# Optimization experiments

Hardware: AMD Instinct MI355X
Metric: run time of the kernel (lower is better)

The kernel has to match this reference:

```python
import jax, jax.numpy as jnp
import numpy as np

K = 100
TEMPERATURE = 0.1


def setup_inputs() -> dict:
    key = jax.random.key(0)
    k1, k2 = jax.random.split(key)
    x = jax.random.normal(k1, (8, 128, 60, 60), dtype=jnp.float32)
    W = jax.random.normal(k2, (128, 2 * K), dtype=jnp.float32) * 0.02  # torch Linear(k*2, d_model).weight
    b = jnp.zeros((128,), dtype=jnp.float32)
    return {"x": x, "W": W, "b": b}


def reference(x, W, b):
    x0, x1 = jnp.split(x, 2, axis=0)
    n, c, h, w = x0.shape
    hw = h * w
    # n c h w -> n (h w) c
    f0 = jnp.transpose(x0.reshape(n, c, hw), (0, 2, 1))
    f1 = jnp.transpose(x1.reshape(n, c, hw), (0, 2, 1))
    # (f0/sqrt(c)) @ (f1/sqrt(c))^T / T  ==  f0 @ f1^T / (c*T)
    sm = jnp.einsum('nld,nsd->nls', f0, f1) / (c * TEMPERATURE)
    cm = (jax.nn.softmax(sm, axis=1) * jax.nn.softmax(sm, axis=2)).reshape(n, hw * hw)
    _, topi = jax.lax.top_k(cm, K)  # (n, K)
    qindex = topi // hw
    rindex = topi % hw
    coords0 = jnp.stack([qindex % w, qindex // w], axis=-1).astype(jnp.float32) / w  # (n, K, 2) as (x, y)
    coords1 = jnp.stack([rindex % w, rindex // w], axis=-1).astype(jnp.float32) / w
    # create_meshgrid(h, w, normalized=False): (1, h*w, 2) with (x, y), row-major
    gy, gx = jnp.meshgrid(jnp.arange(h), jnp.arange(w), indexing='ij')
    grid = jnp.stack([gx, gy], axis=-1).reshape(1, hw, 2).astype(jnp.float32) / w
    offsets0 = grid[:, :, None, :] - coords0[:, None, :, :]  # (n, hw, K, 2)
    offsets1 = grid[:, :, None, :] - coords1[:, None, :, :]
    emb0 = offsets0.reshape(n, hw, 2 * K) @ W.T + b  # (n, hw, d_model)
    emb1 = offsets1.reshape(n, hw, 2 * K) @ W.T + b
    f0 = f0 + emb0
    f1 = f1 + emb1
    f = jnp.concatenate([f0, f1], axis=0)  # (2n, hw, d)
    # n (h w) d -> n d h w
    return jnp.transpose(f, (0, 2, 1)).reshape(2 * n, c, h, w)
```

## Files before the change

kernel.cpp:

```cpp
#include <hip/hip_runtime.h>

#define HW 3600
#define PADR 3712
#define NF4 900
#define CAP 16384
#define KSEL 100
#define NT 58
typedef unsigned long long U64;

using short8   = __attribute__((ext_vector_type(8))) short;
using float4v  = __attribute__((ext_vector_type(4))) float;
using float16v = __attribute__((ext_vector_type(16))) float;

__device__ __forceinline__ unsigned monof(float f) {
    unsigned b = __float_as_uint(f);
    return (b & 0x80000000u) ? ~b : (b | 0x80000000u);
}
__device__ __forceinline__ float unmonof(unsigned m) {
    return __uint_as_float((m & 0x80000000u) ? (m ^ 0x80000000u) : ~m);
}
__device__ __forceinline__ unsigned short f2bf(float f) {
    unsigned b = __float_as_uint(f);
    return (unsigned short)((b + 0x7FFFu + ((b >> 16) & 1u)) >> 16);
}
__device__ __forceinline__ float bf2f(unsigned short h) {
    return __uint_as_float(((unsigned)h) << 16);
}
__device__ __forceinline__ void async16(const void* g, void* l) {
    __builtin_amdgcn_global_load_lds((const __attribute__((address_space(1))) void*)g,
                                     (__attribute__((address_space(3))) void*)l, 16, 0, 0);
}


__global__ __launch_bounds__(256) void conv_k(
    const float* __restrict__ x,
    unsigned short* __restrict__ hiT, unsigned short* __restrict__ loT)
{
    int b = blockIdx.z, l0 = blockIdx.x * 64, d0 = blockIdx.y * 64;
    __shared__ float t[64][65];
    int tid = threadIdx.x;
#pragma unroll
    for (int r = 0; r < 4; r++) {
        int idx = tid + 256 * r;
        int d = idx >> 4, lq = idx & 15;
        int l = l0 + lq * 4;
        const float* src = x + ((size_t)b * 128 + d0 + d) * HW;
        float4 v;
        if (l + 3 < HW) v = *(const float4*)(src + l);
        else {
            v.x = (l     < HW) ? src[l]     : 0.f;
            v.y = (l + 1 < HW) ? src[l + 1] : 0.f;
            v.z = (l + 2 < HW) ? src[l + 2] : 0.f;
            v.w = (l + 3 < HW) ? src[l + 3] : 0.f;
        }
        t[lq * 4 + 0][d] = v.x; t[lq * 4 + 1][d] = v.y;
        t[lq * 4 + 2][d] = v.z; t[lq * 4 + 3][d] = v.w;
    }
    __syncthreads();
    const int rblk = l0 >> 7;
#pragma unroll
    for (int r = 0; r < 2; r++) {
        int idx = tid + 256 * r;
        int l = idx >> 3, dq = idx & 7;
        unsigned hp[4], lp[4];
#pragma unroll
        for (int j = 0; j < 4; j++) {
            float f0 = t[l][dq * 8 + 2 * j], f1 = t[l][dq * 8 + 2 * j + 1];
            unsigned short h0 = f2bf(f0), h1 = f2bf(f1);
            unsigned short g0 = f2bf(f0 - bf2f(h0)), g1 = f2bf(f1 - bf2f(h1));
            hp[j] = (unsigned)h0 | ((unsigned)h1 << 16);
            lp[j] = (unsigned)g0 | ((unsigned)g1 << 16);
        }
        size_t o = ((size_t)(b * 29 + rblk) * 16 + (d0 >> 3) + dq) * 1024
                 + (size_t)((l0 + l) & 127) * 8;
        *(uint4*)(hiT + o) = make_uint4(hp[0], hp[1], hp[2], hp[3]);
        *(uint4*)(loT + o) = make_uint4(lp[0], lp[1], lp[2], lp[3]);
    }
}

__global__ __launch_bounds__(256) void gemm_mfma_k(
    const unsigned short* __restrict__ hiT, const unsigned short* __restrict__ loT,
    float* __restrict__ den_row, float* __restrict__ den_col,
    U64* __restrict__ rowmax, float* __restrict__ maxvt)
{
    const int batch = blockIdx.z, bx = blockIdx.x, by = blockIdx.y;
    __shared__ __align__(16) unsigned short stage[4][4][128][8];
    __shared__ float rowsumS[128], colsumS[128];
    __shared__ U64 rowmaxS[128];

    const int tid = threadIdx.x;
    const int lane = tid & 63, w = tid >> 6;
    const int wr = w >> 1, wc = w & 1;
    const int l31 = lane & 31, h = lane >> 5;

    if (tid < 128) { rowsumS[tid] = 0.f; colsumS[tid] = 0.f; rowmaxS[tid] = 0ull; }

    const unsigned short* psrc = (w == 0) ? hiT : (w == 1) ? loT : (w == 2) ? hiT : loT;
    const int bsel = (w < 2) ? batch : batch + 4;
    const int rblk = (w < 2) ? by : bx;
    const size_t cbase = ((size_t)(bsel * 29 + rblk) * 16) * 1024;

    float16v acc[2][2];
#pragma unroll
    for (int i = 0; i < 2; i++)
#pragma unroll
        for (int j = 0; j < 2; j++) acc[i][j] = (float16v)(0.f);

    for (int k0 = 0; k0 < 128; k0 += 32) {
#pragma unroll
        for (int i = 0; i < 8; i++) {
            int kb = i >> 1, half = i & 1;
            const unsigned short* g = psrc + cbase + (size_t)((k0 >> 3) + kb) * 1024
                                    + (half << 9) + lane * 8;
            async16(g, &stage[w][kb][half << 6][0]);
        }
        __syncthreads();
#pragma unroll
        for (int j = 0; j < 2; j++) {
            int kb = j * 2 + h;
            short8 ah[2], al[2], bh[2], bl[2];
#pragma unroll
            for (int t = 0; t < 2; t++) {
                ah[t] = *(const short8*)&stage[0][kb][wr * 64 + t * 32 + l31][0];
                al[t] = *(const short8*)&stage[1][kb][wr * 64 + t * 32 + l31][0];
                bh[t] = *(const short8*)&stage[2][kb][wc * 64 + t * 32 + l31][0];
                bl[t] = *(const short8*)&stage[3][kb][wc * 64 + t * 32 + l31][0];
            }
#pragma unroll
            for (int mt = 0; mt < 2; mt++)
#pragma unroll
                for (int nt = 0; nt < 2; nt++) {
                    acc[mt][nt] = __builtin_amdgcn_mfma_f32_32x32x16_bf16(ah[mt], bh[nt], acc[mt][nt], 0, 0, 0);
                    acc[mt][nt] = __builtin_amdgcn_mfma_f32_32x32x16_bf16(ah[mt], bl[nt], acc[mt][nt], 0, 0, 0);
                    acc[mt][nt] = __builtin_amdgcn_mfma_f32_32x32x16_bf16(al[mt], bh[nt], acc[mt][nt], 0, 0, 0);
                }
        }
        __syncthreads();
    }

    const float scale = 0.078125f;
    float cs[2] = {0.f, 0.f};
    const int ct = bx * 2 + wc;
#pragma unroll
    for (int mt = 0; mt < 2; mt++) {
#pragma unroll
        for (int reg = 0; reg < 16; reg++) {
            int rloc = (reg & 3) + 8 * (reg >> 2) + 4 * h;
            int row128 = wr * 64 + mt * 32 + rloc;
            int l = by * 128 + row128;
            bool lv = (l < HW);
            float rs = 0.f; U64 pk = 0ull;
#pragma unroll
            for (int nt = 0; nt < 2; nt++) {
                int s = bx * 128 + wc * 64 + nt * 32 + l31;
                float v = acc[mt][nt][reg] * scale;
                if (s < HW) {
                    float e = __expf(v);
                    rs += e;
                    if (lv) cs[nt] += e;
                    U64 k = ((U64)monof(v) << 32) | (unsigned)s;
                    if (k > pk) pk = k;
                }
            }
#pragma unroll
            for (int off = 1; off < 32; off <<= 1) {
                rs += __shfl_xor(rs, off);
                U64 o = __shfl_xor(pk, off);
                if (o > pk) pk = o;
            }
            if (l31 == 0) {
                atomicAdd(&rowsumS[row128], rs);
                atomicMax(&rowmaxS[row128], pk);
                if (lv) maxvt[((size_t)batch * NT + ct) * PADR + l] =
                            unmonof((unsigned)(pk >> 32));
            }
        }
    }
#pragma unroll
    for (int nt = 0; nt < 2; nt++) {
        cs[nt] += __shfl_xor(cs[nt], 32);
        if (h == 0) atomicAdd(&colsumS[wc * 64 + nt * 32 + l31], cs[nt]);
    }
    __syncthreads();
    if (tid < 128) {
        int l = by * 128 + tid;
        if (l < HW) {
            atomicAdd(&den_row[(size_t)batch * HW + l], rowsumS[tid]);
            atomicMax(&rowmax[(size_t)batch * HW + l], rowmaxS[tid]);
        }
        int s = bx * 128 + tid;
        if (s < HW) atomicAdd(&den_col[(size_t)batch * HW + s], colsumS[tid]);
    }
}

__global__ __launch_bounds__(256) void prep_k(
    const float* __restrict__ den_row, const float* __restrict__ den_col,
    const U64* __restrict__ rowmax,
    float* __restrict__ lnDr, float* __restrict__ lnDc,
    float* __restrict__ minlnc, float* __restrict__ tau)
{
    const int batch = blockIdx.z;
    const int tid = threadIdx.x;
    __shared__ float ldrS[HW];
    __shared__ float lncS[HW];
    __shared__ unsigned keyS[HW];
    __shared__ unsigned hist[4096];
    __shared__ unsigned pc[256];
    __shared__ U64 list[HW];
    __shared__ int cntS, binS;
    __shared__ float tauS;

    for (int i = tid; i < HW; i += 256) {
        float ldr = __logf(den_row[(size_t)batch * HW + i]);
        float ldc = __logf(den_col[(size_t)batch * HW + i]);
        lnDr[(size_t)batch * HW + i] = ldr;
        lnDc[(size_t)batch * HW + i] = ldc;
        ldrS[i] = ldr; lncS[i] = ldc;
    }
    for (int i = tid; i < 4096; i += 256) hist[i] = 0u;
    if (tid == 0) cntS = 0;
    __syncthreads();

    if (tid < NT) {
        float mn = 3.4e38f;
        int s0 = tid * 64, s1 = s0 + 64; if (s1 > HW) s1 = HW;
        for (int s = s0; s < s1; s++) mn = fminf(mn, lncS[s]);
        minlnc[batch * NT + tid] = mn;
    }
    for (int i = tid; i < HW; i += 256) {
        U64 rm = rowmax[(size_t)batch * HW + i];
        float mv = unmonof((unsigned)(rm >> 32));
        unsigned col = (unsigned)(rm & 0xffffffffu);
        unsigned km = monof(2.0f * mv - ldrS[i] - lncS[col]);
        keyS[i] = km;
        atomicAdd(&hist[km >> 20], 1u);
    }
    __syncthreads();
    {
        unsigned s = 0;
        for (int j = 0; j < 16; j++) s += hist[tid * 16 + j];
        pc[tid] = s;
    }
    __syncthreads();
    if (tid == 0) {
        unsigned cum = 0; int cs_ = 255;
        for (; cs_ >= 0; cs_--) {
            if (cum + pc[cs_] >= (unsigned)KSEL) break;
            cum += pc[cs_];
        }
        int b = cs_ * 16 + 15;
        for (; b >= cs_ * 16; b--) { cum += hist[b]; if (cum >= (unsigned)KSEL) break; }
        if (b < cs_ * 16) b = cs_ * 16;
        binS = b;
    }
    __syncthreads();
    unsigned bstar = (unsigned)binS;
    for (int i = tid; i < HW; i += 256)
        if ((keyS[i] >> 20) >= bstar) {
            int p = atomicAdd(&cntS, 1);
            list[p] = ((U64)keyS[i] << 32) | (unsigned)(HW - i);
        }
    __syncthreads();
    int Mr = cntS;
    for (int i = tid; i < Mr; i += 256) {
        U64 e = list[i];
        int r = 0;
        for (int j = 0; j < Mr; j++) r += (list[j] > e) ? 1 : 0;
        if (r == KSEL - 1) tauS = unmonof((unsigned)(e >> 32));
    }
    __syncthreads();
    if (tid == 0) tau[batch] = tauS - 1e-4f;
}

__global__ __launch_bounds__(256) void pairs_k(
    const float* __restrict__ maxvt, const float* __restrict__ lnDr,
    const float* __restrict__ minlnc, const float* __restrict__ tau,
    int* __restrict__ pairrows, int* __restrict__ paircnt)
{
    const int batch = blockIdx.z, t = blockIdx.x;
    const float tv = tau[batch] - 1e-4f;
    const float ml = minlnc[batch * NT + t];
    const float* mv = maxvt + ((size_t)batch * NT + t) * PADR;
    const float* ldr = lnDr + (size_t)batch * HW;
    int* pr = pairrows + ((size_t)batch * NT + t) * PADR;
    for (int r = threadIdx.x; r < HW; r += 256) {
        float b = 2.0f * mv[r] - ldr[r] - ml;
        if (b >= tv) {
            int p = atomicAdd(&paircnt[batch * NT + t], 1);
            pr[p] = r;
        }
    }
}

__global__ __launch_bounds__(256) void recollect_k(
    const unsigned short* __restrict__ hiT, const unsigned short* __restrict__ loT,
    const float* __restrict__ lnDr, const float* __restrict__ lnDc,
    const float* __restrict__ tau, const int* __restrict__ pairrows,
    const int* __restrict__ paircnt, uint2* __restrict__ cand,
    int* __restrict__ cnt)
{
    const int t = blockIdx.x, batch = blockIdx.y;
    const int pc = paircnt[batch * NT + t];
    if (pc == 0) return;
    const float tv = tau[batch];
    const int* pr = pairrows + ((size_t)batch * NT + t) * PADR;

    const unsigned short* Ah = hiT + (size_t)batch * PADR * 128;
    const unsigned short* Al = loT + (size_t)batch * PADR * 128;
    const unsigned short* Bh = hiT + (size_t)(batch + 4) * PADR * 128;
    const unsigned short* Bl = loT + (size_t)(batch + 4) * PADR * 128;

    const int tid = threadIdx.x;
    const int lane = tid & 63, w = tid >> 6;
    const int m = lane & 15, q = lane >> 4;
    const float scale = 0.078125f;

    for (int g = w; g * 16 < pc; g += 4) {
        int pi = g * 16 + m;
        int rowv = (pi < pc) ? pr[pi] : HW;
        float ldrv = (pi < pc) ? lnDr[(size_t)batch * HW + rowv] : 0.f;
        size_t arow = ((size_t)(rowv >> 7) * 16) * 1024 + (size_t)(rowv & 127) * 8;

        float4v acc[4];
#pragma unroll
        for (int i = 0; i < 4; i++) acc[i] = (float4v){0.f, 0.f, 0.f, 0.f};
#pragma unroll
        for (int k0 = 0; k0 < 128; k0 += 32) {
            int kb = (k0 >> 3) + q;
            short8 ah = *(const short8*)(Ah + arow + (size_t)kb * 1024);
            short8 al = *(const short8*)(Al + arow + (size_t)kb * 1024);
#pragma unroll
            for (int nt = 0; nt < 4; nt++) {
                int c = t * 64 + nt * 16 + m;
                size_t brow = ((size_t)(c >> 7) * 16 + kb) * 1024 + (size_t)(c & 127) * 8;
                short8 bh = *(const short8*)(Bh + brow);
                short8 bl = *(const short8*)(Bl + brow);
                acc[nt] = __builtin_amdgcn_mfma_f32_16x16x32_bf16(ah, bh, acc[nt], 0, 0, 0);
                acc[nt] = __builtin_amdgcn_mfma_f32_16x16x32_bf16(ah, bl, acc[nt], 0, 0, 0);
                acc[nt] = __builtin_amdgcn_mfma_f32_16x16x32_bf16(al, bh, acc[nt], 0, 0, 0);
            }
        }
#pragma unroll
        for (int nt = 0; nt < 4; nt++) {
            int c = t * 64 + nt * 16 + m;
            if (c >= HW) continue;
            float ldc = lnDc[(size_t)batch * HW + c];
#pragma unroll
            for (int r = 0; r < 4; r++) {
                int ri = q * 4 + r;
                if (g * 16 + ri >= pc) continue;
                int rowo = __shfl(rowv, ri);
                float ldro = __shfl(ldrv, ri);
                float v = acc[nt][r] * scale;
                float tt = 2.0f * v - ldro - ldc;
                if (tt >= tv) {
                    int p = atomicAdd(&cnt[batch], 1);
                    if (p < CAP)
                        cand[(size_t)batch * CAP + p] =
                            make_uint2(monof(tt), (unsigned)(rowo * HW + c));
                }
            }
        }
    }
}

__global__ __launch_bounds__(256) void select_k(
    const uint2* __restrict__ cand, const int* __restrict__ cnt,
    const float* __restrict__ W,
    float* __restrict__ C0, float* __restrict__ C1,
    float* __restrict__ Sx, float* __restrict__ Sy)
{
    const int batch = blockIdx.z;
    const int tid = threadIdx.x;
    const uint2* cb = cand + (size_t)batch * CAP;
    int M = cnt[batch]; if (M > CAP) M = CAP;

    __shared__ U64 lk[6144];
    __shared__ int topiS[KSEL];
    __shared__ float cx0S[KSEL], cy0S[KSEL], cx1S[KSEL], cy1S[KSEL];

    const bool useL = (M <= 6144);
    if (useL)
        for (int i = tid; i < M; i += 256) {
            uint2 e = cb[i];
            lk[i] = ((U64)e.x << 32) | (unsigned)(~e.y);
        }
    __syncthreads();

    for (int i = tid; i < M; i += 256) {
        U64 e;
        if (useL) e = lk[i];
        else { uint2 t = cb[i]; e = ((U64)t.x << 32) | (unsigned)(~t.y); }
        int r = 0;
        for (int j = 0; j < M; j++) {
            U64 o;
            if (useL) o = lk[j];
            else { uint2 t = cb[j]; o = ((U64)t.x << 32) | (unsigned)(~t.y); }
            r += (o > e) ? 1 : 0;
        }
        if (r < KSEL) topiS[r] = (int)(~(unsigned)(e & 0xffffffffu));
    }
    __syncthreads();

    if (tid < KSEL) {
        int idx = topiS[tid];
        int qq = idx / HW, rr = idx - qq * HW;
        cx0S[tid] = (float)(qq % 60) / 60.0f;
        cy0S[tid] = (float)(qq / 60) / 60.0f;
        cx1S[tid] = (float)(rr % 60) / 60.0f;
        cy1S[tid] = (float)(rr / 60) / 60.0f;
    }
    __syncthreads();
    if (tid < 128) {
        const float* wr_ = W + tid * 200;
        float c0 = 0.f, c1 = 0.f, sx = 0.f, sy = 0.f;
        for (int k = 0; k < KSEL; k++) {
            float wx = wr_[2 * k], wy = wr_[2 * k + 1];
            c0 += cx0S[k] * wx + cy0S[k] * wy;
            c1 += cx1S[k] * wx + cy1S[k] * wy;
            sx += wx; sy += wy;
        }
        C0[batch * 128 + tid] = c0;
        C1[batch * 128 + tid] = c1;
        if (batch == 0) { Sx[tid] = sx; Sy[tid] = sy; }
    }
}

__global__ __launch_bounds__(256) void final_k(
    const float* __restrict__ x, const float* __restrict__ bias,
    const float* __restrict__ C0, const float* __restrict__ C1,
    const float* __restrict__ Sx, const float* __restrict__ Sy,
    float* __restrict__ out)
{
    int bd = blockIdx.x;
    int b = bd >> 7, d = bd & 127;
    float cst = bias[d] - ((b < 4) ? C0[b * 128 + d] : C1[(b - 4) * 128 + d]);
    float sx = Sx[d], sy = Sy[d];
    const float4* xin = (const float4*)(x + (size_t)bd * HW);
    float4* o4 = (float4*)(out + (size_t)bd * HW);
    for (int f = threadIdx.x; f < NF4; f += 256) {
        float4 v = xin[f];
        int p0 = f * 4;
        float gy = (float)(p0 / 60) / 60.0f;
        float gxb = (float)(p0 % 60);
        float add = cst + gy * sy;
        v.x += add + ((gxb       ) / 60.0f) * sx;
        v.y += add + ((gxb + 1.f) / 60.0f) * sx;
        v.z += add + ((gxb + 2.f) / 60.0f) * sx;
        v.w += add + ((gxb + 3.f) / 60.0f) * sx;
        o4[f] = v;
    }
}

extern "C" void kernel_launch(void* const* d_in, const int* in_sizes, int n_in,
                              void* d_out, int out_size, void* d_ws, size_t ws_size,
                              hipStream_t stream)
{
    const float* x    = (const float*)d_in[0];
    const float* W    = (const float*)d_in[1];
    const float* bias = (const float*)d_in[2];
    float* out = (float*)d_out;

    char* ws = (char*)d_ws;
    float*    den_row = (float*)(ws + 0);
    float*    den_col = (float*)(ws + 57600);
    U64*      rowmax  = (U64*)  (ws + 115200);
    int*      cnt     = (int*)  (ws + 230400);
    float*    tau     = (float*)(ws + 230416);
    float*    lnDr    = (float*)(ws + 230464);
    float*    lnDc    = (float*)(ws + 288064);
    float*    minlnc  = (float*)(ws + 345664);
    int*      paircnt = (int*)  (ws + 346592);
    float*    C0      = (float*)(ws + 347584);
    float*    C1      = (float*)(ws + 349632);
    float*    Sx      = (float*)(ws + 351680);
    float*    Sy      = (float*)(ws + 352192);
    uint2*    cand    = (uint2*)(ws + 352768);
    int*      pairrows= (int*)  (ws + 877056);
    float*    maxvt   = (float*)(ws + 4321792);
    unsigned short* hiT = (unsigned short*)(ws + 7766528);
    unsigned short* loT = (unsigned short*)(ws + 15368704);

    hipMemsetAsync(ws, 0, 230432, stream);
    hipMemsetAsync(ws + 346592, 0, 928, stream);

    conv_k     <<<dim3(58, 2, 8),  256, 0, stream>>>(x, hiT, loT);
    gemm_mfma_k<<<dim3(29, 29, 4), 256, 0, stream>>>(hiT, loT, den_row, den_col, rowmax, maxvt);
    prep_k     <<<dim3(1, 1, 4),   256, 0, stream>>>(den_row, den_col, rowmax, lnDr, lnDc, minlnc, tau);
    pairs_k    <<<dim3(NT, 1, 4),  256, 0, stream>>>(maxvt, lnDr, minlnc, tau, pairrows, paircnt);
    recollect_k<<<dim3(NT, 4),     256, 0, stream>>>(hiT, loT, lnDr, lnDc, tau, pairrows, paircnt, cand, cnt);
    select_k   <<<dim3(1, 1, 4),   256, 0, stream>>>(cand, cnt, W, C0, C1, Sx, Sy);
    final_k    <<<dim3(1024),      256, 0, stream>>>(x, bias, C0, C1, Sx, Sy, out);
}
```

Measured before the change: 266.4 us.

## Replace single-block prep with parallel log/tile-stat/lower-bound kernels and radix top-k selection

Removes the 64-bit packed row max and its atomics from the GEMM epilogue, keeping only per-tile float maxima. The serial one-block prep kernel is split into parallel kernels: a logarithm pass, a per-tile min/max of log column sums, and a per-row key lower bound built from tile maxima. The threshold and the final top-k are then found with a two-level radix histogram instead of O(M^2) rank counting. The conv_k store index is also remapped for better write coalescing. The looser lower-bound threshold (margin widened to 3e-4) may admit more candidates and adds launches.

```diff
diff --git a/kernel.cpp b/kernel.cpp
--- a/kernel.cpp
+++ b/kernel.cpp
@@ -61,7 +61,7 @@
 #pragma unroll
     for (int r = 0; r < 2; r++) {
         int idx = tid + 256 * r;
-        int l = idx >> 3, dq = idx & 7;
+        int l = idx & 63, dq = idx >> 6;
         unsigned hp[4], lp[4];
 #pragma unroll
         for (int j = 0; j < 4; j++) {
@@ -81,19 +81,18 @@
 __global__ __launch_bounds__(256) void gemm_mfma_k(
     const unsigned short* __restrict__ hiT, const unsigned short* __restrict__ loT,
     float* __restrict__ den_row, float* __restrict__ den_col,
-    U64* __restrict__ rowmax, float* __restrict__ maxvt)
+    float* __restrict__ maxvt)
 {
     const int batch = blockIdx.z, bx = blockIdx.x, by = blockIdx.y;
     __shared__ __align__(16) unsigned short stage[4][4][128][8];
     __shared__ float rowsumS[128], colsumS[128];
-    __shared__ U64 rowmaxS[128];
 
     const int tid = threadIdx.x;
     const int lane = tid & 63, w = tid >> 6;
     const int wr = w >> 1, wc = w & 1;
     const int l31 = lane & 31, h = lane >> 5;
 
-    if (tid < 128) { rowsumS[tid] = 0.f; colsumS[tid] = 0.f; rowmaxS[tid] = 0ull; }
+    if (tid < 128) { rowsumS[tid] = 0.f; colsumS[tid] = 0.f; }
 
     const unsigned short* psrc = (w == 0) ? hiT : (w == 1) ? loT : (w == 2) ? hiT : loT;
     const int bsel = (w < 2) ? batch : batch + 4;
@@ -149,7 +148,7 @@
             int row128 = wr * 64 + mt * 32 + rloc;
             int l = by * 128 + row128;
             bool lv = (l < HW);
-            float rs = 0.f; U64 pk = 0ull;
+            float rs = 0.f, mx = -3.4e38f;
 #pragma unroll
             for (int nt = 0; nt < 2; nt++) {
                 int s = bx * 128 + wc * 64 + nt * 32 + l31;
@@ -158,21 +157,17 @@
                     float e = __expf(v);
                     rs += e;
                     if (lv) cs[nt] += e;
-                    U64 k = ((U64)monof(v) << 32) | (unsigned)s;
-                    if (k > pk) pk = k;
+                    mx = fmaxf(mx, v);
                 }
             }
 #pragma unroll
             for (int off = 1; off < 32; off <<= 1) {
                 rs += __shfl_xor(rs, off);
-                U64 o = __shfl_xor(pk, off);
-                if (o > pk) pk = o;
+                mx = fmaxf(mx, __shfl_xor(mx, off));
             }
             if (l31 == 0) {
                 atomicAdd(&rowsumS[row128], rs);
-                atomicMax(&rowmaxS[row128], pk);
-                if (lv) maxvt[((size_t)batch * NT + ct) * PADR + l] =
-                            unmonof((unsigned)(pk >> 32));
+                if (lv) maxvt[((size_t)batch * NT + ct) * PADR + l] = mx;
             }
         }
     }
@@ -184,92 +179,122 @@
     __syncthreads();
     if (tid < 128) {
         int l = by * 128 + tid;
-        if (l < HW) {
-            atomicAdd(&den_row[(size_t)batch * HW + l], rowsumS[tid]);
-            atomicMax(&rowmax[(size_t)batch * HW + l], rowmaxS[tid]);
-        }
+        if (l < HW) atomicAdd(&den_row[(size_t)batch * HW + l], rowsumS[tid]);
         int s = bx * 128 + tid;
         if (s < HW) atomicAdd(&den_col[(size_t)batch * HW + s], colsumS[tid]);
     }
 }
 
-__global__ __launch_bounds__(256) void prep_k(
-    const float* __restrict__ den_row, const float* __restrict__ den_col,
-    const U64* __restrict__ rowmax,
-    float* __restrict__ lnDr, float* __restrict__ lnDc,
-    float* __restrict__ minlnc, float* __restrict__ tau)
-{
-    const int batch = blockIdx.z;
-    const int tid = threadIdx.x;
-    __shared__ float ldrS[HW];
-    __shared__ float lncS[HW];
+__global__ __launch_bounds__(256) void logs_k(
+    const float* __restrict__ den, float* __restrict__ lnD)
+{
+    int i = blockIdx.x * 256 + threadIdx.x;
+    if (i < 28800) lnD[i] = __logf(den[i]);
+}
+
+__global__ __launch_bounds__(64) void tilestat_k(
+    const float* __restrict__ lnDc, float* __restrict__ minlnc, float* __restrict__ maxlnc)
+{
+    int t = blockIdx.x, b = blockIdx.z, tid = threadIdx.x;
+    int j = t * 64 + tid;
+    float v = (j < HW) ? lnDc[(size_t)b * HW + j] : 0.f;
+    float mn = (j < HW) ? v : 3.4e38f;
+    float mx = (j < HW) ? v : -3.4e38f;
+#pragma unroll
+    for (int off = 1; off < 64; off <<= 1) {
+        mn = fminf(mn, __shfl_xor(mn, off));
+        mx = fmaxf(mx, __shfl_xor(mx, off));
+    }
+    if (tid == 0) {
+        if (mx == -3.4e38f) { mx = 1e30f; mn = 1e30f; }
+        minlnc[b * NT + t] = mn;
+        maxlnc[b * NT + t] = mx;
+    }
+}
+
+__global__ __launch_bounds__(256) void keylb_k(
+    const float* __restrict__ maxvt, const float* __restrict__ lnDr,
+    const float* __restrict__ maxlnc, float* __restrict__ keylb)
+{
+    int b = blockIdx.z, j = blockIdx.x * 256 + threadIdx.x;
+    __shared__ float mls[NT];
+    if (threadIdx.x < NT) mls[threadIdx.x] = maxlnc[b * NT + threadIdx.x];
+    __syncthreads();
+    if (j >= HW) return;
+    float best = -3.4e38f;
+#pragma unroll 2
+    for (int t = 0; t < NT; t++) {
+        float v = maxvt[((size_t)b * NT + t) * PADR + j];
+        best = fmaxf(best, 2.0f * v - mls[t]);
+    }
+    keylb[(size_t)b * HW + j] = best - lnDr[(size_t)b * HW + j];
+}
+
+__global__ __launch_bounds__(256) void tau_k(
+    const float* __restrict__ keylb, float* __restrict__ tau)
+{
+    const int b = blockIdx.z, tid = threadIdx.x;
     __shared__ unsigned keyS[HW];
     __shared__ unsigned hist[4096];
     __shared__ unsigned pc[256];
-    __shared__ U64 list[HW];
-    __shared__ int cntS, binS;
-    __shared__ float tauS;
-
+    __shared__ int b1S, c1S, b2S, lcnt;
+    __shared__ unsigned bestS;
+    __shared__ unsigned list[1024];
+
+    for (int i = tid; i < 4096; i += 256) hist[i] = 0u;
+    if (tid == 0) { lcnt = 0; bestS = 0u; }
+    __syncthreads();
     for (int i = tid; i < HW; i += 256) {
-        float ldr = __logf(den_row[(size_t)batch * HW + i]);
-        float ldc = __logf(den_col[(size_t)batch * HW + i]);
-        lnDr[(size_t)batch * HW + i] = ldr;
-        lnDc[(size_t)batch * HW + i] = ldc;
-        ldrS[i] = ldr; lncS[i] = ldc;
-    }
-    for (int i = tid; i < 4096; i += 256) hist[i] = 0u;
-    if (tid == 0) cntS = 0;
-    __syncthreads();
-
-    if (tid < NT) {
-        float mn = 3.4e38f;
-        int s0 = tid * 64, s1 = s0 + 64; if (s1 > HW) s1 = HW;
-        for (int s = s0; s < s1; s++) mn = fminf(mn, lncS[s]);
-        minlnc[batch * NT + tid] = mn;
-    }
-    for (int i = tid; i < HW; i += 256) {
-        U64 rm = rowmax[(size_t)batch * HW + i];
-        float mv = unmonof((unsigned)(rm >> 32));
-        unsigned col = (unsigned)(rm & 0xffffffffu);
-        unsigned km = monof(2.0f * mv - ldrS[i] - lncS[col]);
-        keyS[i] = km;
-        atomicAdd(&hist[km >> 20], 1u);
-    }
-    __syncthreads();
-    {
-        unsigned s = 0;
-        for (int j = 0; j < 16; j++) s += hist[tid * 16 + j];
-        pc[tid] = s;
-    }
+        unsigned k = monof(keylb[(size_t)b * HW + i]);
+        keyS[i] = k;
+        atomicAdd(&hist[k >> 20], 1u);
+    }
+    __syncthreads();
+    { unsigned s = 0; for (int j = 0; j < 16; j++) s += hist[tid * 16 + j]; pc[tid] = s; }
     __syncthreads();
     if (tid == 0) {
         unsigned cum = 0; int cs_ = 255;
-        for (; cs_ >= 0; cs_--) {
-            if (cum + pc[cs_] >= (unsigned)KSEL) break;
-            cum += pc[cs_];
-        }
-        int b = cs_ * 16 + 15;
-        for (; b >= cs_ * 16; b--) { cum += hist[b]; if (cum >= (unsigned)KSEL) break; }
-        if (b < cs_ * 16) b = cs_ * 16;
-        binS = b;
-    }
-    __syncthreads();
-    unsigned bstar = (unsigned)binS;
-    for (int i = tid; i < HW; i += 256)
-        if ((keyS[i] >> 20) >= bstar) {
-            int p = atomicAdd(&cntS, 1);
-            list[p] = ((U64)keyS[i] << 32) | (unsigned)(HW - i);
-        }
-    __syncthreads();
-    int Mr = cntS;
-    for (int i = tid; i < Mr; i += 256) {
-        U64 e = list[i];
-        int r = 0;
-        for (int j = 0; j < Mr; j++) r += (list[j] > e) ? 1 : 0;
-        if (r == KSEL - 1) tauS = unmonof((unsigned)(e >> 32));
-    }
-    __syncthreads();
-    if (tid == 0) tau[batch] = tauS - 1e-4f;
+        for (; cs_ > 0; cs_--) { if (cum + pc[cs_] >= (unsigned)KSEL) break; cum += pc[cs_]; }
+        int bb = cs_ * 16 + 15;
+        for (; bb > cs_ * 16; bb--) { if (cum + hist[bb] >= (unsigned)KSEL) break; cum += hist[bb]; }
+        b1S = bb; c1S = (int)cum;
+    }
+    __syncthreads();
+    int b1 = b1S;
+    for (int i = tid; i < 4096; i += 256) hist[i] = 0u;
+    __syncthreads();
+    for (int i = tid; i < HW; i += 256) {
+        unsigned k = keyS[i];
+        if ((int)(k >> 20) == b1) atomicAdd(&hist[(k >> 8) & 4095], 1u);
+    }
+    __syncthreads();
+    { unsigned s = 0; for (int j = 0; j < 16; j++) s += hist[tid * 16 + j]; pc[tid] = s; }
+    __syncthreads();
+    if (tid == 0) {
+        unsigned cum = (unsigned)c1S; int cs_ = 255;
+        for (; cs_ > 0; cs_--) { if (cum + pc[cs_] >= (unsigned)KSEL) break; cum += pc[cs_]; }
+        int bb = cs_ * 16 + 15;
+        for (; bb > cs_ * 16; bb--) { if (cum + hist[bb] >= (unsigned)KSEL) break; cum += hist[bb]; }
+        b2S = bb;
+    }
+    __syncthreads();
+    int b2 = b2S;
+    for (int i = tid; i < HW; i += 256) {
+        unsigned k = keyS[i]; int hb = (int)(k >> 20);
+        if (hb > b1 || (hb == b1 && (int)((k >> 8) & 4095) >= b2)) {
+            int p = atomicAdd(&lcnt, 1);
+            if (p < 1024) list[p] = k;
+        }
+    }
+    __syncthreads();
+    int L = lcnt; if (L > 1024) L = 1024;
+    for (int i = tid; i < L; i += 256) {
+        unsigned e = list[i]; int c = 0;
+        for (int j = 0; j < L; j++) c += (list[j] >= e) ? 1 : 0;
+        if (c >= KSEL) atomicMax(&bestS, e);
+    }
+    __syncthreads();
+    if (tid == 0) tau[b] = unmonof(bestS) - 3e-4f;
 }
 
 __global__ __launch_bounds__(256) void pairs_k(
@@ -278,7 +303,7 @@
     int* __restrict__ pairrows, int* __restrict__ paircnt)
 {
     const int batch = blockIdx.z, t = blockIdx.x;
-    const float tv = tau[batch] - 1e-4f;
+    const float tv = tau[batch] - 3e-4f;
     const float ml = minlnc[batch * NT + t];
     const float* mv = maxvt + ((size_t)batch * NT + t) * PADR;
     const float* ldr = lnDr + (size_t)batch * HW;
@@ -370,34 +395,64 @@
     float* __restrict__ C0, float* __restrict__ C1,
     float* __restrict__ Sx, float* __restrict__ Sy)
 {
-    const int batch = blockIdx.z;
-    const int tid = threadIdx.x;
+    const int batch = blockIdx.z, tid = threadIdx.x;
     const uint2* cb = cand + (size_t)batch * CAP;
     int M = cnt[batch]; if (M > CAP) M = CAP;
 
-    __shared__ U64 lk[6144];
+    __shared__ unsigned hist[4096];
+    __shared__ unsigned pc[256];
+    __shared__ int b1S, c1S, b2S, lcnt;
+    __shared__ U64 list[512];
     __shared__ int topiS[KSEL];
     __shared__ float cx0S[KSEL], cy0S[KSEL], cx1S[KSEL], cy1S[KSEL];
 
-    const bool useL = (M <= 6144);
-    if (useL)
-        for (int i = tid; i < M; i += 256) {
-            uint2 e = cb[i];
-            lk[i] = ((U64)e.x << 32) | (unsigned)(~e.y);
-        }
-    __syncthreads();
-
+    for (int i = tid; i < 4096; i += 256) hist[i] = 0u;
+    if (tid == 0) lcnt = 0;
+    __syncthreads();
+    for (int i = tid; i < M; i += 256) atomicAdd(&hist[cb[i].x >> 20], 1u);
+    __syncthreads();
+    { unsigned s = 0; for (int j = 0; j < 16; j++) s += hist[tid * 16 + j]; pc[tid] = s; }
+    __syncthreads();
+    if (tid == 0) {
+        unsigned cum = 0; int cs_ = 255;
+        for (; cs_ > 0; cs_--) { if (cum + pc[cs_] >= (unsigned)KSEL) break; cum += pc[cs_]; }
+        int bb = cs_ * 16 + 15;
+        for (; bb > cs_ * 16; bb--) { if (cum + hist[bb] >= (unsigned)KSEL) break; cum += hist[bb]; }
+        b1S = bb; c1S = (int)cum;
+    }
+    __syncthreads();
+    int b1 = b1S;
+    for (int i = tid; i < 4096; i += 256) hist[i] = 0u;
+    __syncthreads();
     for (int i = tid; i < M; i += 256) {
-        U64 e;
-        if (useL) e = lk[i];
-        else { uint2 t = cb[i]; e = ((U64)t.x << 32) | (unsigned)(~t.y); }
-        int r = 0;
-        for (int j = 0; j < M; j++) {
-            U64 o;
-            if (useL) o = lk[j];
-            else { uint2 t = cb[j]; o = ((U64)t.x << 32) | (unsigned)(~t.y); }
-            r += (o > e) ? 1 : 0;
-        }
+        unsigned k = cb[i].x;
+        if ((int)(k >> 20) == b1) atomicAdd(&hist[(k >> 8) & 4095], 1u);
+    }
+    __syncthreads();
+    { unsigned s = 0; for (int j = 0; j < 16; j++) s += hist[tid * 16 + j]; pc[tid] = s; }
+    __syncthreads();
+    if (tid == 0) {
+        unsigned cum = (unsigned)c1S; int cs_ = 255;
+        for (; cs_ > 0; cs_--) { if (cum + pc[cs_] >= (unsigned)KSEL) break; cum += pc[cs_]; }
+        int bb = cs_ * 16 + 15;
+        for (; bb > cs_ * 16; bb--) { if (cum + hist[bb] >= (unsigned)KSEL) break; cum += hist[bb]; }
+        b2S = bb;
+    }
+    __syncthreads();
+    int b2 = b2S;
+    for (int i = tid; i < M; i += 256) {
+        uint2 e = cb[i];
+        int hb = (int)(e.x >> 20);
+        if (hb > b1 || (hb == b1 && (int)((e.x >> 8) & 4095) >= b2)) {
+            int p = atomicAdd(&lcnt, 1);
+            if (p < 512) list[p] = ((U64)e.x << 32) | (unsigned)(~e.y);
+        }
+    }
+    __syncthreads();
+    int L = lcnt; if (L > 512) L = 512;
+    for (int i = tid; i < L; i += 256) {
+        U64 e = list[i]; int r = 0;
+        for (int j = 0; j < L; j++) r += (list[j] > e) ? 1 : 0;
         if (r < KSEL) topiS[r] = (int)(~(unsigned)(e & 0xffffffffu));
     }
     __syncthreads();
@@ -462,31 +517,38 @@
     float* out = (float*)d_out;
 
     char* ws = (char*)d_ws;
-    float*    den_row = (float*)(ws + 0);
+    float*    den     = (float*)(ws + 0);
+    float*    den_row = den;
     float*    den_col = (float*)(ws + 57600);
-    U64*      rowmax  = (U64*)  (ws + 115200);
+    float*    lnD     = (float*)(ws + 115200);
+    float*    lnDr    = lnD;
+    float*    lnDc    = (float*)(ws + 172800);
     int*      cnt     = (int*)  (ws + 230400);
     float*    tau     = (float*)(ws + 230416);
-    float*    lnDr    = (float*)(ws + 230464);
-    float*    lnDc    = (float*)(ws + 288064);
-    float*    minlnc  = (float*)(ws + 345664);
-    int*      paircnt = (int*)  (ws + 346592);
-    float*    C0      = (float*)(ws + 347584);
-    float*    C1      = (float*)(ws + 349632);
-    float*    Sx      = (float*)(ws + 351680);
-    float*    Sy      = (float*)(ws + 352192);
-    uint2*    cand    = (uint2*)(ws + 352768);
-    int*      pairrows= (int*)  (ws + 877056);
-    float*    maxvt   = (float*)(ws + 4321792);
-    unsigned short* hiT = (unsigned short*)(ws + 7766528);
-    unsigned short* loT = (unsigned short*)(ws + 15368704);
-
-    hipMemsetAsync(ws, 0, 230432, stream);
-    hipMemsetAsync(ws + 346592, 0, 928, stream);
+    float*    minlnc  = (float*)(ws + 230432);
+    float*    maxlnc  = (float*)(ws + 231360);
+    int*      paircnt = (int*)  (ws + 232288);
+    float*    keylb   = (float*)(ws + 233216);
+    float*    C0      = (float*)(ws + 290816);
+    float*    C1      = (float*)(ws + 292864);
+    float*    Sx      = (float*)(ws + 294912);
+    float*    Sy      = (float*)(ws + 295424);
+    uint2*    cand    = (uint2*)(ws + 295936);
+    int*      pairrows= (int*)  (ws + 820224);
+    float*    maxvt   = (float*)(ws + 4264960);
+    unsigned short* hiT = (unsigned short*)(ws + 7709696);
+    unsigned short* loT = (unsigned short*)(ws + 15311872);
+
+    hipMemsetAsync(ws, 0, 115200, stream);
+    hipMemsetAsync(ws + 230400, 0, 32, stream);
+    hipMemsetAsync(ws + 232288, 0, 928, stream);
 
     conv_k     <<<dim3(58, 2, 8),  256, 0, stream>>>(x, hiT, loT);
-    gemm_mfma_k<<<dim3(29, 29, 4), 256, 0, stream>>>(hiT, loT, den_row, den_col, rowmax, maxvt);
-    prep_k     <<<dim3(1, 1, 4),   256, 0, stream>>>(den_row, den_col, rowmax, lnDr, lnDc, minlnc, tau);
+    gemm_mfma_k<<<dim3(29, 29, 4), 256, 0, stream>>>(hiT, loT, den_row, den_col, maxvt);
+    logs_k     <<<dim3(113),       256, 0, stream>>>(den, lnD);
+    tilestat_k <<<dim3(NT, 1, 4),   64, 0, stream>>>(lnDc, minlnc, maxlnc);
+    keylb_k    <<<dim3(15, 1, 4),  256, 0, stream>>>(maxvt, lnDr, maxlnc, keylb);
+    tau_k      <<<dim3(1, 1, 4),   256, 0, stream>>>(keylb, tau);
     pairs_k    <<<dim3(NT, 1, 4),  256, 0, stream>>>(maxvt, lnDr, minlnc, tau, pairrows, paircnt);
     recollect_k<<<dim3(NT, 4),     256, 0, stream>>>(hiT, loT, lnDr, lnDc, tau, pairrows, paircnt, cand, cnt);
     select_k   <<<dim3(1, 1, 4),   256, 0, stream>>>(cand, cnt, W, C0, C1, Sx, Sy);
```

New measurement: 263.0 us. About the same (-1.3%).
